# Kernel optimization log

Hardware: AMD Instinct MI355X
Metric: run time of the kernel (lower is better)

The kernel has to match this reference:

```python
import jax, jax.numpy as jnp
import numpy as np

B, S, D, H = 4, 2048, 512, 8
DH = D // H  # depth per head = 64


def setup_inputs() -> dict:
    key = jax.random.key(0)
    ks = jax.random.split(key, 8)
    scale = 1.0 / np.sqrt(D)
    return {
        "query": jax.random.normal(ks[0], (B, S, D), jnp.float32),
        "key": jax.random.normal(ks[1], (B, S, D), jnp.float32),
        "value": jax.random.normal(ks[2], (B, S, D), jnp.float32),
        "mask": jax.random.randint(ks[3], (B, S), 0, 2, jnp.int32),
        "wq_w": jax.random.normal(ks[4], (D, D), jnp.float32) * scale,
        "wq_b": jnp.zeros((D,), jnp.float32),
        "wk_w": jax.random.normal(ks[5], (D, D), jnp.float32) * scale,
        "wk_b": jnp.zeros((D,), jnp.float32),
        "wv_w": jax.random.normal(ks[6], (D, D), jnp.float32) * scale,
        "wv_b": jnp.zeros((D,), jnp.float32),
        "wo_w": jax.random.normal(ks[7], (D, D), jnp.float32) * scale,
        "wo_b": jnp.zeros((D,), jnp.float32),
    }


def _split_heads(x):
    # [B, S, D] -> [B, H, S, DH]
    b, s, _ = x.shape
    return x.reshape(b, s, H, DH).transpose(0, 2, 1, 3)


def reference(query, key, value, mask, wq_w, wq_b, wk_w, wk_b, wv_w, wv_b, wo_w, wo_b):
    q = _split_heads(query @ wq_w + wq_b)   # [B,H,S,DH]
    k = _split_heads(key @ wk_w + wk_b)
    v = _split_heads(value @ wv_w + wv_b)

    scale = 1.0 / jnp.sqrt(jnp.asarray(DH, jnp.float32))
    logits = jnp.einsum('bhqd,bhkd->bhqk', q, k) * scale  # [B,H,S,S]
    # additive key-padding mask: 1 -> masked (adds -1e9)
    m = mask.astype(logits.dtype)[:, None, None, :]  # [B,1,1,S]
    logits = logits + m * -1e9
    weights = jax.nn.softmax(logits, axis=-1)
    attn = jnp.einsum('bhqk,bhkd->bhqd', weights, v)  # [B,H,S,DH]
    attn = attn.transpose(0, 2, 1, 3).reshape(query.shape[0], -1, D)  # [B,S,D]
    return attn @ wo_w + wo_b
```

## Files before the change

### kernel.cpp

```cpp
#include <hip/hip_runtime.h>
#include <stdint.h>

#define QSCALE (0.125f * 1.44269504088896340736f)
#define MASKNEG (-1.442695e9f)

typedef unsigned short u16;
typedef unsigned int u32;
typedef __bf16 bf16x8 __attribute__((ext_vector_type(8)));
typedef float f32x4 __attribute__((ext_vector_type(4)));
typedef float f32x16 __attribute__((ext_vector_type(16)));
typedef u16 u16x8 __attribute__((ext_vector_type(8)));
typedef u32 u32x4 __attribute__((ext_vector_type(4)));

__device__ __forceinline__ u16 f2bf(float f) {
  u32 u = __float_as_uint(f);
  u += 0x7fffu + ((u >> 16) & 1u);
  return (u16)(u >> 16);
}

__device__ __forceinline__ u32 cvtpk(float lo, float hi) {
  u32 d;
  asm("v_cvt_pk_bf16_f32 %0, %1, %2" : "=v"(d) : "v"(lo), "v"(hi));
  return d;
}

__device__ __forceinline__ void plswap(u32& a, u32& b) {
  asm("v_permlane32_swap_b32 %0, %1" : "+v"(a), "+v"(b));
}

__device__ __forceinline__ void gload16(const void* src, void* ldsbase) {
  __builtin_amdgcn_global_load_lds(
      (const __attribute__((address_space(1))) u32*)src,
      (__attribute__((address_space(3))) u32*)ldsbase, 16, 0, 0);
}

__global__ __launch_bounds__(256) void conv_in(const float* __restrict__ q,
                                               const float* __restrict__ k,
                                               const float* __restrict__ v,
                                               u16* __restrict__ dst) {
  const float* src = (blockIdx.z == 0) ? q : (blockIdx.z == 1) ? k : v;
  u16* d = dst + (size_t)blockIdx.z * 4194304;
  size_t i = ((size_t)blockIdx.x * 256 + threadIdx.x) * 8;
  float4 a = *(const float4*)(src + i);
  float4 b = *(const float4*)(src + i + 4);
  u16x8 ov;
  ov[0] = f2bf(a.x); ov[1] = f2bf(a.y); ov[2] = f2bf(a.z); ov[3] = f2bf(a.w);
  ov[4] = f2bf(b.x); ov[5] = f2bf(b.y); ov[6] = f2bf(b.z); ov[7] = f2bf(b.w);
  *(u16x8*)(d + i) = ov;
}

__global__ __launch_bounds__(256) void conv_w(const float* __restrict__ wq,
                                              const float* __restrict__ wk,
                                              const float* __restrict__ wv,
                                              const float* __restrict__ wo,
                                              u16* __restrict__ wT) {
  const float* src = (blockIdx.z == 0) ? wq : (blockIdx.z == 1) ? wk
                    : (blockIdx.z == 2) ? wv : wo;
  u16* dst = wT + (size_t)blockIdx.z * 262144;
  __shared__ float t[64][65];
  const int n0 = blockIdx.x * 64, k0 = blockIdx.y * 64;
  const int lr = threadIdx.x >> 6, lc = threadIdx.x & 63;
#pragma unroll
  for (int it = 0; it < 16; ++it) {
    const int row = it * 4 + lr;
    t[row][lc] = src[(size_t)(k0 + row) * 512 + n0 + lc];
  }
  __syncthreads();
#pragma unroll
  for (int it = 0; it < 16; ++it) {
    const int row = it * 4 + lr;
    dst[(size_t)(n0 + row) * 512 + k0 + lc] = f2bf(t[lc][row]);
  }
}

__device__ __forceinline__ void gemm_core(const u16* __restrict__ A,
                                          const u16* __restrict__ Bt,
                                          int m0, int n0, char* lds,
                                          f32x4 acc[4][4]) {
  const int tid = threadIdx.x;
  const int lane = tid & 63;
  const int wave = tid >> 6;
  const int wm = wave >> 1, wn = wave & 1;
  const int srow = tid >> 3;
  const int sc16 = tid & 7;

  auto stage = [&](int buf, int kt) {
    const int k0 = kt * 64;
    char* base = lds + buf * 32768;
#pragma unroll
    for (int c = 0; c < 4; ++c) {
      const int row = c * 32 + srow;
      const int xc = (sc16 ^ (row & 7)) << 3;
      gload16(A + (size_t)(m0 + row) * 512 + k0 + xc,
              base + c * 4096 + (wave << 10));
      gload16(Bt + (size_t)(n0 + row) * 512 + k0 + xc,
              base + 16384 + c * 4096 + (wave << 10));
    }
  };

  auto compute = [&](int buf) {
    const char* bA = lds + buf * 32768;
    const char* bB = bA + 16384;
#pragma unroll
    for (int kk = 0; kk < 2; ++kk) {
      const int c16 = kk * 4 + (lane >> 4);
      bf16x8 av[4], bv[4];
#pragma unroll
      for (int i = 0; i < 4; ++i) {
        const int row = wm * 64 + i * 16 + (lane & 15);
        av[i] = *(const bf16x8*)(bA + row * 128 + ((c16 ^ (row & 7)) << 4));
      }
#pragma unroll
      for (int j = 0; j < 4; ++j) {
        const int row = wn * 64 + j * 16 + (lane & 15);
        bv[j] = *(const bf16x8*)(bB + row * 128 + ((c16 ^ (row & 7)) << 4));
      }
#pragma unroll
      for (int i = 0; i < 4; ++i)
#pragma unroll
        for (int j = 0; j < 4; ++j)
          acc[i][j] = __builtin_amdgcn_mfma_f32_16x16x32_bf16(av[i], bv[j],
                                                              acc[i][j], 0, 0, 0);
    }
  };

  stage(0, 0);
  __syncthreads();
#pragma unroll
  for (int kt = 0; kt < 8; ++kt) {
    const int cur = kt & 1;
    if (kt < 7) stage(cur ^ 1, kt + 1);
    compute(cur);
    __syncthreads();
  }
}

__global__ __launch_bounds__(256) void gemm_qkv(
    const u16* __restrict__ xq, const u16* __restrict__ xk,
    const u16* __restrict__ xv, const u16* __restrict__ wT,
    const float* __restrict__ bq, const float* __restrict__ bk,
    const float* __restrict__ bv, u16* __restrict__ qws, u16* __restrict__ kws,
    u16* __restrict__ vTw) {
  __shared__ __align__(16) char lds[65536];
  const int z = blockIdx.z;
  const u16* A = (z == 0) ? xq : (z == 1) ? xk : xv;
  const u16* Bt = wT + (size_t)z * 262144;
  const float* bias = (z == 0) ? bq : (z == 1) ? bk : bv;
  const int m0 = blockIdx.y * 128, n0 = blockIdx.x * 128;
  f32x4 acc[4][4] = {};
  gemm_core(A, Bt, m0, n0, lds, acc);
  const int lane = threadIdx.x & 63, wave = threadIdx.x >> 6;
  const int wm = wave >> 1, wn = wave & 1;
#pragma unroll
  for (int j = 0; j < 4; ++j) {
    const int n = n0 + wn * 64 + j * 16 + (lane & 15);
    const float bn = bias[n];
    const int h = n >> 6, dh = n & 63;
#pragma unroll
    for (int i = 0; i < 4; ++i) {
#pragma unroll
      for (int r = 0; r < 4; ++r) {
        const int rg = m0 + wm * 64 + i * 16 + ((lane >> 4) << 2) + r;
        const int b = rg >> 11, s = rg & 2047;
        const int bh = b * 8 + h;
        const float val = acc[i][j][r] + bn;
        if (z == 0) {
          qws[((size_t)bh * 2048 + s) * 64 + dh] = f2bf(val * QSCALE);
        } else if (z == 1) {
          kws[((size_t)bh * 2048 + s) * 64 + dh] = f2bf(val);
        } else {
          vTw[((size_t)bh * 64 + dh) * 2048 + s] = f2bf(val);
        }
      }
    }
  }
}

__global__ __launch_bounds__(512, 4) void attn_fwd(
    const u16* __restrict__ qws, const u16* __restrict__ kws,
    const u16* __restrict__ vTw, const int* __restrict__ mask,
    u16* __restrict__ attn) {
  __shared__ __align__(16) char ldsK[32768];
  __shared__ __align__(16) char ldsV[32768];
  __shared__ __align__(16) float biasLDS[2048];
  __shared__ float lSh[256];

  const int bh = blockIdx.x;
  const int qt = blockIdx.y;
  const int b = bh >> 3;
  const int tid = threadIdx.x;
  const int lane = tid & 63, wave = tid >> 6;
  const int half = wave >> 2, wl = wave & 3;
  const int l31 = lane & 31, h5 = lane >> 5;

  {
    const int4 m4 = *(const int4*)(mask + b * 2048 + tid * 4);
    float4 bv;
    bv.x = m4.x ? MASKNEG : 0.0f;
    bv.y = m4.y ? MASKNEG : 0.0f;
    bv.z = m4.z ? MASKNEG : 0.0f;
    bv.w = m4.w ? MASKNEG : 0.0f;
    *(float4*)(biasLDS + tid * 4) = bv;
  }
  asm volatile("s_waitcnt lgkmcnt(0)" ::: "memory");

  const u16* qrow_p = qws + ((size_t)bh * 2048 + qt * 128 + wl * 32 + l31) * 64;
  bf16x8 qb[4];
#pragma unroll
  for (int c = 0; c < 4; ++c)
    qb[c] = *(const bf16x8*)(qrow_p + c * 16 + h5 * 8);

  const int rowb = l31 * 128;
  int kxs[4];
#pragma unroll
  for (int c = 0; c < 4; ++c) kxs[c] = ((2 * c + h5) ^ (l31 & 7)) << 4;

  char* myK = ldsK + half * 16384;
  char* myV = ldsV + half * 16384;
  const int srow = wl * 8 + (lane >> 3);
  const int sc16 = lane & 7;

  auto stage = [&](int buf, int ktg) {
#pragma unroll
    for (int c = 0; c < 2; ++c) {
      const int row = c * 32 + srow;
      const int xc = (sc16 ^ (row & 7)) << 3;
      gload16(kws + ((size_t)bh * 2048 + ktg * 64 + row) * 64 + xc,
              myK + buf * 8192 + c * 4096 + (wl << 10));
      gload16(vTw + ((size_t)bh * 64 + row) * 2048 + ktg * 64 + xc,
              myV + buf * 8192 + c * 4096 + (wl << 10));
    }
  };

  f32x16 o0 = {}, o1 = {};
  float rsp0 = 0.f, rsp1 = 0.f, rsp2 = 0.f, rsp3 = 0.f;

  auto do_subtile = [&](const char* kb, const char* vb, const float* biasT,
                        int stByte, int c0) {
    f32x16 sv;
#pragma unroll
    for (int g = 0; g < 4; ++g) {
      const f32x4 bq4 = *(const f32x4*)(biasT + g * 8 + h5 * 4);
      sv[g * 4 + 0] = bq4[0];
      sv[g * 4 + 1] = bq4[1];
      sv[g * 4 + 2] = bq4[2];
      sv[g * 4 + 3] = bq4[3];
    }
    __builtin_amdgcn_s_setprio(1);
#pragma unroll
    for (int c = 0; c < 4; ++c) {
      const bf16x8 kf = *(const bf16x8*)(kb + stByte + rowb + kxs[c]);
      sv = __builtin_amdgcn_mfma_f32_32x32x16_bf16(kf, qb[c], sv, 0, 0, 0);
    }
    __builtin_amdgcn_s_setprio(0);
    float p[16];
#pragma unroll
    for (int i = 0; i < 16; ++i) p[i] = __builtin_amdgcn_exp2f(sv[i]);
    rsp0 += p[0] + p[4] + p[8] + p[12];
    rsp1 += p[1] + p[5] + p[9] + p[13];
    rsp2 += p[2] + p[6] + p[10] + p[14];
    rsp3 += p[3] + p[7] + p[11] + p[15];
    u32 paw[2][4];
#pragma unroll
    for (int lc = 0; lc < 2; ++lc) {
      u32 a1 = cvtpk(p[lc * 8 + 0], p[lc * 8 + 1]);
      u32 b1 = cvtpk(p[lc * 8 + 4], p[lc * 8 + 5]);
      u32 a2 = cvtpk(p[lc * 8 + 2], p[lc * 8 + 3]);
      u32 b2 = cvtpk(p[lc * 8 + 6], p[lc * 8 + 7]);
      plswap(a1, b1);
      plswap(a2, b2);
      paw[lc][0] = a1; paw[lc][1] = a2; paw[lc][2] = b1; paw[lc][3] = b2;
    }
    __builtin_amdgcn_s_setprio(1);
#pragma unroll
    for (int lc = 0; lc < 2; ++lc) {
      u32x4 w = {paw[lc][0], paw[lc][1], paw[lc][2], paw[lc][3]};
      const bf16x8 pa = __builtin_bit_cast(bf16x8, w);
      const bf16x8 vf0 = *(const bf16x8*)(vb + rowb + kxs[c0 + lc]);
      o0 = __builtin_amdgcn_mfma_f32_32x32x16_bf16(pa, vf0, o0, 0, 0, 0);
      const bf16x8 vf1 = *(const bf16x8*)(vb + 4096 + rowb + kxs[c0 + lc]);
      o1 = __builtin_amdgcn_mfma_f32_32x32x16_bf16(pa, vf1, o1, 0, 0, 0);
    }
    __builtin_amdgcn_s_setprio(0);
  };

  stage(0, half * 16);

  for (int kt = 0; kt < 16; ++kt) {
    const int cur = kt & 1;
    const int ktg = half * 16 + kt;
    if (kt < 15) {
      stage(cur ^ 1, ktg + 1);
      asm volatile("s_waitcnt vmcnt(4)" ::: "memory");
    } else {
      asm volatile("s_waitcnt vmcnt(0)" ::: "memory");
    }
    __builtin_amdgcn_sched_barrier(0);
    __builtin_amdgcn_s_barrier();
    const char* kb = myK + cur * 8192;
    const char* vb = myV + cur * 8192;
    const float* biasT = biasLDS + ktg * 64;
    do_subtile(kb, vb, biasT, 0, 0);
    do_subtile(kb, vb, biasT + 32, 4096, 2);
    __builtin_amdgcn_sched_barrier(0);
    __builtin_amdgcn_s_barrier();
  }

  float rs = (rsp0 + rsp1) + (rsp2 + rsp3);
  rs += __shfl_xor(rs, 32);

  float* oSh = (float*)(half ? (void*)ldsV : (void*)ldsK);
#pragma unroll
  for (int reg = 0; reg < 16; ++reg) {
    const int q = (reg & 3) + 8 * (reg >> 2) + 4 * h5;
    oSh[wl * 2048 + q * 64 + l31] = o0[reg];
    oSh[wl * 2048 + q * 64 + 32 + l31] = o1[reg];
  }
  if (h5 == 0) lSh[half * 128 + wl * 32 + l31] = rs;
  __syncthreads();

  const int h = bh & 7;
#pragma unroll
  for (int i = 0; i < 2; ++i) {
    const int idx = tid + i * 512;
    const int row = idx >> 3;
    const int c8 = (idx & 7) * 8;
    const float inv = 1.0f / (lSh[row] + lSh[128 + row]);
    const float* A = (const float*)ldsK + row * 64 + c8;
    const float* Bp = (const float*)ldsV + row * 64 + c8;
    u16x8 ovv;
#pragma unroll
    for (int j = 0; j < 8; ++j) ovv[j] = f2bf((A[j] + Bp[j]) * inv);
    const int grow = b * 2048 + qt * 128 + row;
    *(u16x8*)(attn + (size_t)grow * 512 + h * 64 + c8) = ovv;
  }
}

__global__ __launch_bounds__(256) void gemm_out(const u16* __restrict__ attn,
                                                const u16* __restrict__ woT,
                                                const float* __restrict__ bo,
                                                float* __restrict__ out) {
  __shared__ __align__(16) char lds[65536];
  const int m0 = blockIdx.y * 128, n0 = blockIdx.x * 128;
  f32x4 acc[4][4] = {};
  gemm_core(attn, woT, m0, n0, lds, acc);
  const int lane = threadIdx.x & 63, wave = threadIdx.x >> 6;
  const int wm = wave >> 1, wn = wave & 1;
#pragma unroll
  for (int j = 0; j < 4; ++j) {
    const int n = n0 + wn * 64 + j * 16 + (lane & 15);
    const float bn = bo[n];
#pragma unroll
    for (int i = 0; i < 4; ++i) {
      const int rbase = m0 + wm * 64 + i * 16 + ((lane >> 4) << 2);
#pragma unroll
      for (int r = 0; r < 4; ++r)
        out[(size_t)(rbase + r) * 512 + n] = acc[i][j][r] + bn;
    }
  }
}

extern "C" void kernel_launch(void* const* d_in, const int* in_sizes, int n_in,
                              void* d_out, int out_size, void* d_ws,
                              size_t ws_size, hipStream_t stream) {
  (void)in_sizes; (void)n_in; (void)out_size; (void)ws_size;
  const float* q = (const float*)d_in[0];
  const float* k = (const float*)d_in[1];
  const float* v = (const float*)d_in[2];
  const int* mask = (const int*)d_in[3];
  const float* wq = (const float*)d_in[4];
  const float* bq = (const float*)d_in[5];
  const float* wk = (const float*)d_in[6];
  const float* bk = (const float*)d_in[7];
  const float* wv = (const float*)d_in[8];
  const float* bv = (const float*)d_in[9];
  const float* wo = (const float*)d_in[10];
  const float* bo = (const float*)d_in[11];

  u16* xq = (u16*)d_ws;
  u16* xk = xq + 4194304;
  u16* xv = xk + 4194304;
  u16* wT = xv + 4194304;
  u16* qws = wT + 1048576;
  u16* kws = qws + 4194304;
  u16* vTw = kws + 4194304;
  u16* attn = xq;
  float* out = (float*)d_out;

  conv_in<<<dim3(2048, 1, 3), 256, 0, stream>>>(q, k, v, xq);
  conv_w<<<dim3(8, 8, 4), 256, 0, stream>>>(wq, wk, wv, wo, wT);
  gemm_qkv<<<dim3(4, 64, 3), 256, 0, stream>>>(xq, xk, xv, wT, bq, bk, bv, qws,
                                               kws, vTw);
  attn_fwd<<<dim3(32, 16), 512, 0, stream>>>(qws, kws, vTw, mask, attn);
  gemm_out<<<dim3(4, 64), 256, 0, stream>>>(attn, wT + 786432, bo, out);
}
```

Baseline: 104.4 us.

## Fuse fp32-to-bf16 input conversion into QKV GEMM and restructure attention epilogue

```diff
diff --git a/kernel.cpp b/kernel.cpp
--- a/kernel.cpp
+++ b/kernel.cpp
@@ -32,21 +32,6 @@
   __builtin_amdgcn_global_load_lds(
       (const __attribute__((address_space(1))) u32*)src,
       (__attribute__((address_space(3))) u32*)ldsbase, 16, 0, 0);
-}
-
-__global__ __launch_bounds__(256) void conv_in(const float* __restrict__ q,
-                                               const float* __restrict__ k,
-                                               const float* __restrict__ v,
-                                               u16* __restrict__ dst) {
-  const float* src = (blockIdx.z == 0) ? q : (blockIdx.z == 1) ? k : v;
-  u16* d = dst + (size_t)blockIdx.z * 4194304;
-  size_t i = ((size_t)blockIdx.x * 256 + threadIdx.x) * 8;
-  float4 a = *(const float4*)(src + i);
-  float4 b = *(const float4*)(src + i + 4);
-  u16x8 ov;
-  ov[0] = f2bf(a.x); ov[1] = f2bf(a.y); ov[2] = f2bf(a.z); ov[3] = f2bf(a.w);
-  ov[4] = f2bf(b.x); ov[5] = f2bf(b.y); ov[6] = f2bf(b.z); ov[7] = f2bf(b.w);
-  *(u16x8*)(d + i) = ov;
 }
 
 __global__ __launch_bounds__(256) void conv_w(const float* __restrict__ wq,
@@ -73,10 +58,22 @@
   }
 }
 
-__device__ __forceinline__ void gemm_core(const u16* __restrict__ A,
-                                          const u16* __restrict__ Bt,
-                                          int m0, int n0, char* lds,
-                                          f32x4 acc[4][4]) {
+__global__ __launch_bounds__(256) void gemm_qkv(
+    const float* __restrict__ xqf, const float* __restrict__ xkf,
+    const float* __restrict__ xvf, const u16* __restrict__ wT,
+    const float* __restrict__ bq, const float* __restrict__ bk,
+    const float* __restrict__ bv, u16* __restrict__ qws, u16* __restrict__ kws,
+    u16* __restrict__ vTw) {
+  __shared__ __align__(16) char lds[65536];
+  const int hw = blockIdx.x;
+  const int lg = (hw & 7) * 96 + (hw >> 3);
+  const int z = lg >> 8;
+  const int rem = lg & 255;
+  const int m0 = (rem >> 2) * 128, n0 = (rem & 3) * 128;
+  const float* A = (z == 0) ? xqf : (z == 1) ? xkf : xvf;
+  const u16* Bt = wT + (size_t)z * 262144;
+  const float* bias = (z == 0) ? bq : (z == 1) ? bk : bv;
+
   const int tid = threadIdx.x;
   const int lane = tid & 63;
   const int wave = tid >> 6;
@@ -84,17 +81,41 @@
   const int srow = tid >> 3;
   const int sc16 = tid & 7;
 
-  auto stage = [&](int buf, int kt) {
+  f32x4 acc[4][4] = {};
+
+  auto stageB = [&](int buf, int kt) {
     const int k0 = kt * 64;
-    char* base = lds + buf * 32768;
+    char* base = lds + buf * 32768 + 16384;
 #pragma unroll
     for (int c = 0; c < 4; ++c) {
       const int row = c * 32 + srow;
       const int xc = (sc16 ^ (row & 7)) << 3;
-      gload16(A + (size_t)(m0 + row) * 512 + k0 + xc,
+      gload16(Bt + (size_t)(n0 + row) * 512 + k0 + xc,
               base + c * 4096 + (wave << 10));
-      gload16(Bt + (size_t)(n0 + row) * 512 + k0 + xc,
-              base + 16384 + c * 4096 + (wave << 10));
+    }
+  };
+
+  auto stageA_load = [&](int kt, float4* ld) {
+    const int k0 = kt * 64;
+#pragma unroll
+    for (int c = 0; c < 4; ++c) {
+      const int row = c * 32 + srow;
+      const float* sp = A + (size_t)(m0 + row) * 512 + k0 + sc16 * 8;
+      ld[c * 2] = *(const float4*)sp;
+      ld[c * 2 + 1] = *(const float4*)(sp + 4);
+    }
+  };
+
+  auto stageA_write = [&](int buf, const float4* ld) {
+    char* base = lds + buf * 32768;
+#pragma unroll
+    for (int c = 0; c < 4; ++c) {
+      const int row = c * 32 + srow;
+      const float4 a = ld[c * 2], d = ld[c * 2 + 1];
+      u16x8 w;
+      w[0] = f2bf(a.x); w[1] = f2bf(a.y); w[2] = f2bf(a.z); w[3] = f2bf(a.w);
+      w[4] = f2bf(d.x); w[5] = f2bf(d.y); w[6] = f2bf(d.z); w[7] = f2bf(d.w);
+      *(u16x8*)(base + row * 128 + ((sc16 ^ (row & 7)) << 4)) = w;
     }
   };
 
@@ -124,33 +145,26 @@
     }
   };
 
-  stage(0, 0);
+  {
+    float4 ld[8];
+    stageA_load(0, ld);
+    stageB(0, 0);
+    stageA_write(0, ld);
+  }
   __syncthreads();
 #pragma unroll
   for (int kt = 0; kt < 8; ++kt) {
     const int cur = kt & 1;
-    if (kt < 7) stage(cur ^ 1, kt + 1);
+    float4 nld[8];
+    if (kt < 7) {
+      stageA_load(kt + 1, nld);
+      stageB(cur ^ 1, kt + 1);
+    }
     compute(cur);
+    if (kt < 7) stageA_write(cur ^ 1, nld);
     __syncthreads();
   }
-}
-
-__global__ __launch_bounds__(256) void gemm_qkv(
-    const u16* __restrict__ xq, const u16* __restrict__ xk,
-    const u16* __restrict__ xv, const u16* __restrict__ wT,
-    const float* __restrict__ bq, const float* __restrict__ bk,
-    const float* __restrict__ bv, u16* __restrict__ qws, u16* __restrict__ kws,
-    u16* __restrict__ vTw) {
-  __shared__ __align__(16) char lds[65536];
-  const int z = blockIdx.z;
-  const u16* A = (z == 0) ? xq : (z == 1) ? xk : xv;
-  const u16* Bt = wT + (size_t)z * 262144;
-  const float* bias = (z == 0) ? bq : (z == 1) ? bk : bv;
-  const int m0 = blockIdx.y * 128, n0 = blockIdx.x * 128;
-  f32x4 acc[4][4] = {};
-  gemm_core(A, Bt, m0, n0, lds, acc);
-  const int lane = threadIdx.x & 63, wave = threadIdx.x >> 6;
-  const int wm = wave >> 1, wn = wave & 1;
+
 #pragma unroll
   for (int j = 0; j < 4; ++j) {
     const int n = n0 + wn * 64 + j * 16 + (lane & 15);
@@ -183,7 +197,7 @@
   __shared__ __align__(16) char ldsK[32768];
   __shared__ __align__(16) char ldsV[32768];
   __shared__ __align__(16) float biasLDS[2048];
-  __shared__ float lSh[256];
+  __shared__ float lShA[128];
 
   const int bh = blockIdx.x;
   const int qt = blockIdx.y;
@@ -309,30 +323,40 @@
   float rs = (rsp0 + rsp1) + (rsp2 + rsp3);
   rs += __shfl_xor(rs, 32);
 
-  float* oSh = (float*)(half ? (void*)ldsV : (void*)ldsK);
-#pragma unroll
-  for (int reg = 0; reg < 16; ++reg) {
-    const int q = (reg & 3) + 8 * (reg >> 2) + 4 * h5;
-    oSh[wl * 2048 + q * 64 + l31] = o0[reg];
-    oSh[wl * 2048 + q * 64 + 32 + l31] = o1[reg];
-  }
-  if (h5 == 0) lSh[half * 128 + wl * 32 + l31] = rs;
+  float* oSh2 = (float*)ldsK;
+  u16* trb = (u16*)ldsV;
+  if (half == 1) {
+#pragma unroll
+    for (int reg = 0; reg < 16; ++reg) {
+      oSh2[(wl * 32 + reg) * 64 + lane] = o0[reg];
+      oSh2[(wl * 32 + 16 + reg) * 64 + lane] = o1[reg];
+    }
+    if (h5 == 0) lShA[wl * 32 + l31] = rs;
+  }
   __syncthreads();
-
+  if (half == 0) {
+    const float ltot = rs + lShA[wl * 32 + l31];
+    const float linv = 1.0f / ltot;
+#pragma unroll
+    for (int reg = 0; reg < 16; ++reg) {
+      const int q = (reg & 3) + 8 * (reg >> 2) + 4 * h5;
+      const float inv = __shfl(linv, q);
+      const float v0 = (o0[reg] + oSh2[(wl * 32 + reg) * 64 + lane]) * inv;
+      const float v1 = (o1[reg] + oSh2[(wl * 32 + 16 + reg) * 64 + lane]) * inv;
+      trb[(wl * 32 + q) * 64 + l31] = f2bf(v0);
+      trb[(wl * 32 + q) * 64 + 32 + l31] = f2bf(v1);
+    }
+  }
+  __syncthreads();
   const int h = bh & 7;
 #pragma unroll
   for (int i = 0; i < 2; ++i) {
-    const int idx = tid + i * 512;
-    const int row = idx >> 3;
-    const int c8 = (idx & 7) * 8;
-    const float inv = 1.0f / (lSh[row] + lSh[128 + row]);
-    const float* A = (const float*)ldsK + row * 64 + c8;
-    const float* Bp = (const float*)ldsV + row * 64 + c8;
-    u16x8 ovv;
-#pragma unroll
-    for (int j = 0; j < 8; ++j) ovv[j] = f2bf((A[j] + Bp[j]) * inv);
+    const int ii = tid + i * 512;
+    const int row = ii >> 3;
+    const int c8 = (ii & 7) * 8;
+    const u16x8 vv = *(const u16x8*)(trb + row * 64 + c8);
     const int grow = b * 2048 + qt * 128 + row;
-    *(u16x8*)(attn + (size_t)grow * 512 + h * 64 + c8) = ovv;
+    *(u16x8*)(attn + (size_t)grow * 512 + h * 64 + c8) = vv;
   }
 }
 
@@ -341,11 +365,71 @@
                                                 const float* __restrict__ bo,
                                                 float* __restrict__ out) {
   __shared__ __align__(16) char lds[65536];
-  const int m0 = blockIdx.y * 128, n0 = blockIdx.x * 128;
+  const int hw = blockIdx.x;
+  const int lg = (hw & 7) * 32 + (hw >> 3);
+  const int m0 = (lg >> 2) * 128, n0 = (lg & 3) * 128;
+
+  const int tid = threadIdx.x;
+  const int lane = tid & 63;
+  const int wave = tid >> 6;
+  const int wm = wave >> 1, wn = wave & 1;
+  const int srow = tid >> 3;
+  const int sc16 = tid & 7;
+
   f32x4 acc[4][4] = {};
-  gemm_core(attn, woT, m0, n0, lds, acc);
-  const int lane = threadIdx.x & 63, wave = threadIdx.x >> 6;
-  const int wm = wave >> 1, wn = wave & 1;
+
+  auto stage = [&](int buf, int kt) {
+    const int k0 = kt * 64;
+    char* base = lds + buf * 32768;
+#pragma unroll
+    for (int c = 0; c < 4; ++c) {
+      const int row = c * 32 + srow;
+      const int xc = (sc16 ^ (row & 7)) << 3;
+      gload16(attn + (size_t)(m0 + row) * 512 + k0 + xc,
+              base + c * 4096 + (wave << 10));
+      gload16(woT + (size_t)(n0 + row) * 512 + k0 + xc,
+              base + 16384 + c * 4096 + (wave << 10));
+    }
+  };
+
+  auto compute = [&](int buf) {
+    const char* bA = lds + buf * 32768;
+    const char* bB = bA + 16384;
+#pragma unroll
+    for (int kk = 0; kk < 2; ++kk) {
+      const int c16 = kk * 4 + (lane >> 4);
+      bf16x8 av[4], bv[4];
+#pragma unroll
+      for (int i = 0; i < 4; ++i) {
+        const int row = wm * 64 + i * 16 + (lane & 15);
+        av[i] = *(const bf16x8*)(bA + row * 128 + ((c16 ^ (row & 7)) << 4));
+      }
+#pragma unroll
+      for (int j = 0; j < 4; ++j) {
+        const int row = wn * 64 + j * 16 + (lane & 15);
+        bv[j] = *(const bf16x8*)(bB + row * 128 + ((c16 ^ (row & 7)) << 4));
+      }
+#pragma unroll
+      for (int i = 0; i < 4; ++i)
+#pragma unroll
+        for (int j = 0; j < 4; ++j)
+          acc[i][j] = __builtin_amdgcn_mfma_f32_16x16x32_bf16(av[i], bv[j],
+                                                              acc[i][j], 0, 0, 0);
+    }
+  };
+
+  stage(0, 0);
+  __syncthreads();
+#pragma unroll
+  for (int kt = 0; kt < 8; ++kt) {
+    const int cur = kt & 1;
+    if (kt < 7) stage(cur ^ 1, kt + 1);
+    compute(cur);
+    __syncthreads();
+  }
+
+  const float bn_base = 0.f;
+  (void)bn_base;
 #pragma unroll
   for (int j = 0; j < 4; ++j) {
     const int n = n0 + wn * 64 + j * 16 + (lane & 15);
@@ -377,20 +461,15 @@
   const float* wo = (const float*)d_in[10];
   const float* bo = (const float*)d_in[11];
 
-  u16* xq = (u16*)d_ws;
-  u16* xk = xq + 4194304;
-  u16* xv = xk + 4194304;
-  u16* wT = xv + 4194304;
+  u16* attnb = (u16*)d_ws;
+  u16* wT = attnb + 3 * 4194304;
   u16* qws = wT + 1048576;
   u16* kws = qws + 4194304;
   u16* vTw = kws + 4194304;
-  u16* attn = xq;
   float* out = (float*)d_out;
 
-  conv_in<<<dim3(2048, 1, 3), 256, 0, stream>>>(q, k, v, xq);
   conv_w<<<dim3(8, 8, 4), 256, 0, stream>>>(wq, wk, wv, wo, wT);
-  gemm_qkv<<<dim3(4, 64, 3), 256, 0, stream>>>(xq, xk, xv, wT, bq, bk, bv, qws,
-                                               kws, vTw);
-  attn_fwd<<<dim3(32, 16), 512, 0, stream>>>(qws, kws, vTw, mask, attn);
-  gemm_out<<<dim3(4, 64), 256, 0, stream>>>(attn, wT + 786432, bo, out);
-}
+  gemm_qkv<<<768, 256, 0, stream>>>(q, k, v, wT, bq, bk, bv, qws, kws, vTw);
+  attn_fwd<<<dim3(32, 16), 512, 0, stream>>>(qws, kws, vTw, mask, attnb);
+  gemm_out<<<256, 256, 0, stream>>>(attnb, wT + 786432, bo, out);
+}
```

Result: no change. 104.7 us (+0.3%).
